# Kernel optimization log

Hardware: AMD Instinct MI355X
Metric: run time of the kernel (lower is better)

## Reference

```python
import jax, jax.numpy as jnp
import numpy as np


def _cd2(a, b):
    # squared euclidean distances [n,m]
    d = jnp.sum(a * a, 1)[:, None] + jnp.sum(b * b, 1)[None, :] - 2.0 * (a @ b.T)
    return jnp.maximum(d, 0.0)


def _cdist(a, b):
    # tiny clamp keeps sqrt grad finite on the zero diagonal, fwd unchanged
    return jnp.sqrt(jnp.maximum(_cd2(a, b), 1e-30))


def _tmedian(x):
    # torch.median semantics: lower middle element
    f = jnp.sort(x.reshape(-1))
    return f[(f.shape[0] - 1) // 2]


def setup_inputs() -> dict:
    key = jax.random.key(0)
    k1, k2 = jax.random.split(key)
    feat_s = jax.random.normal(k1, (25, 640), dtype=jnp.float32)
    y_s = (jnp.arange(25) % 5).astype(jnp.int32)  # 5-way 5-shot, every class present
    feat_q = jax.random.normal(k2, (300, 640), dtype=jnp.float32)
    return {"feat_s": feat_s, "y_s": y_s, "feat_q": feat_q}


def reference(feat_s, y_s, feat_q):
    y_s_np = np.asarray(y_s)
    classes = np.unique(y_s_np)
    C = int(classes.shape[0])
    onehot = jnp.asarray(y_s_np[:, None] == classes[None, :], dtype=feat_s.dtype)  # [S,C]
    prototypes = (onehot.T @ feat_s) / jnp.sum(onehot, 0)[:, None]  # [C,D]

    # ---- virtual mixup densification ----
    dist_q = _cdist(feat_q, prototypes)  # [Nq,C]
    y_boot = np.asarray(jnp.argmin(dist_q, 1))
    q_norm = feat_q / jnp.linalg.norm(feat_q, axis=1, keepdims=True)
    cos_np = np.asarray(q_norm @ q_norm.T)
    dist_q_np = np.asarray(dist_q)
    virt = []
    for c in range(C):
        idx = np.flatnonzero(y_boot == c)
        if idx.size < 2:
            continue
        cos_c = cos_np[np.ix_(idx, idx)]
        f = np.sort(cos_c.reshape(-1))
        thresh = f[(f.size - 1) // 2]  # torch lower median
        ii, jj = np.nonzero(np.triu(cos_c >= thresh, 1))  # pairs with i<j
        if ii.size:
            virt.append(0.5 * (feat_q[idx[ii]] + feat_q[idx[jj]]))
        kq = int(idx[np.argmin(dist_q_np[idx, c])])
        virt.append((0.5 * (prototypes[c] + feat_q[kq]))[None, :])
    feat_all = jnp.concatenate([feat_q] + virt, 0) if virt else feat_q

    # ---- self-tuning affinity (kNN graph) ----
    n = int(feat_all.shape[0])
    k = max(1, int(np.log2(n)))
    dist = _cdist(feat_all, feat_all)  # [n,n]
    _, nn_idx = jax.lax.top_k(-dist, k + 1)  # smallest k+1 (incl. self)
    sigma = dist[jnp.arange(n), nn_idx[:, k]] + 1e-8
    nbrs = nn_idx[:, 1:]  # [n,k]
    d_nb = jnp.take_along_axis(dist, nbrs, 1)
    w = jnp.exp(-d_nb / (sigma[:, None] * sigma[nbrs]))
    W = jnp.zeros((n, n), feat_all.dtype).at[jnp.arange(n)[:, None], nbrs].set(w)
    W = (W + W.T) / 2
    D_inv = 1.0 / (W.sum(1) + 1e-8)

    # ---- density-adaptive lambda ----
    d = _cdist(feat_all, prototypes).min(1)
    lam = jnp.exp(-(d ** 2) / (2 * _tmedian(d) ** 2 + 1e-8))

    # ---- mm iterations (label propagation) ----
    a = _cd2(feat_all, prototypes)  # [n,C]
    y0 = jax.nn.softmax(-a, axis=1)
    scale = (lam * D_inv)[:, None]

    def step(carry, _):
        y, done = carry
        y_new = jax.nn.softmax(-a + scale * (W @ y), axis=1)
        conv = jnp.max(jnp.abs(y_new - y)) < 1e-4
        y_out = jnp.where(done | conv, y, y_new)  # emulate torch early break
        return (y_out, done | conv), None

    (y, _), _ = jax.lax.scan(step, (y0, jnp.asarray(False)), None, length=50)
    preds = jnp.argmax(y[: feat_q.shape[0]], 1)
    return preds
```

## Files before the change

### kernel.cpp

```cpp
#include <hip/hip_runtime.h>
#include <math.h>

#define CMAX 8
#define KMAX 16
#define TPB 256
#define BNMAX 1024

struct P {
  const float* fs; const int* ys; const float* fq;
  int S, Q, D, BN, NMAX;
  float* proto;
  float* G;
  float* cosq;
  int* ybt;
  int* cls; int* scount; int* qcount; int* qidx; int* kq;
  float* thr;
  int* rowcnt; int* rowoff; int* paircnt; int* basev;
  int* meta;
  int* uv;
  float* rn2;
  float* H;
  int* cand;
  int* nbrs; float* dnb; float* wgt; float* sigma;
  int* indeg; int* inoff; int* cursor;
  int* insrcU; float* inwU; int* indst;
  int* insrc; float* inw;
  unsigned* cosk;
  unsigned* gmaxu;
  float* amat; float* dinv; float* dmin; float* scalev;
  float* yA; float* yB;
  float* meddenom;
  int* outp;
};

__device__ inline unsigned f2key(float f){
  unsigned b=__float_as_uint(f);
  return (b&0x80000000u)? ~b : (b|0x80000000u);
}
__device__ inline float key2f(unsigned k){
  unsigned b=(k&0x80000000u)? (k^0x80000000u) : ~k;
  return __uint_as_float(b);
}
__device__ inline unsigned long long shfl_xor_u64(unsigned long long v,int m){
  unsigned lo=(unsigned)v, hi=(unsigned)(v>>32);
  lo=__shfl_xor(lo,m,64); hi=__shfl_xor(hi,m,64);
  return (((unsigned long long)hi)<<32)|lo;
}

__global__ void k_init(P p){
  if (threadIdx.x==0){
    int labs[CMAX]; int cnt[CMAX]; int C=0;
    for (int s=0;s<p.S;s++){
      int l=p.ys[s]; int f=-1;
      for(int c=0;c<C;c++) if(labs[c]==l){f=c;break;}
      if(f<0){ if(C<CMAX){labs[C]=l;cnt[C]=1;C++;} }
      else cnt[f]++;
    }
    for(int a=0;a<C;a++)for(int b=a+1;b<C;b++)
      if(labs[b]<labs[a]){int t=labs[a];labs[a]=labs[b];labs[b]=t;
                          t=cnt[a];cnt[a]=cnt[b];cnt[b]=t;}
    for(int c=0;c<C;c++){p.cls[c]=labs[c];p.scount[c]=cnt[c];}
    p.meta[0]=C;
  }
}

__global__ void k_proto(P p){
  int c=blockIdx.x; int C=p.meta[0];
  for(int d=threadIdx.x; d<p.D; d+=blockDim.x){
    float s=0.f;
    if(c<C){
      int lab=p.cls[c];
      for(int j=0;j<p.S;j++) if(p.ys[j]==lab) s+=p.fs[(size_t)j*p.D+d];
      s/= (float)p.scount[c];
    }
    p.proto[(size_t)c*p.D+d]=s;
  }
}

__global__ void k_gram(P p){
  __shared__ float arow[1024];
  int a=blockIdx.x;
  const float* ra = (a<p.Q)? p.fq + (size_t)a*p.D : p.proto + (size_t)(a-p.Q)*p.D;
  const float* A = ra;
  if(p.D<=1024){
    for(int d=threadIdx.x; d<p.D; d+=blockDim.x) arow[d]=ra[d];
    __syncthreads();
    A=(const float*)arow;
  }
  int D4=p.D>>2; int Dt=D4<<2;
  for(int b=threadIdx.x; b<p.BN; b+=blockDim.x){
    const float* rb=(b<p.Q)? p.fq+(size_t)b*p.D : p.proto+(size_t)(b-p.Q)*p.D;
    const float4* a4=(const float4*)A;
    const float4* b4=(const float4*)rb;
    float s=0.f;
    #pragma unroll 4
    for(int d=0;d<D4;d++){
      float4 x=a4[d], y=b4[d];
      s += x.x*y.x + x.y*y.y + x.z*y.z + x.w*y.w;
    }
    for(int d=Dt;d<p.D;d++) s += A[d]*rb[d];
    p.G[(size_t)a*p.BN+b]=s;
  }
}

__global__ void k_cos(P p){
  int t=blockIdx.x*blockDim.x+threadIdx.x;
  if(t>=p.Q*p.Q)return;
  int i=t/p.Q, j=t%p.Q;
  p.cosq[t]=p.G[(size_t)i*p.BN+j]/(sqrtf(p.G[(size_t)i*p.BN+i])*sqrtf(p.G[(size_t)j*p.BN+j]));
}

__global__ void k_yboot(P p){
  int q=blockIdx.x*blockDim.x+threadIdx.x;
  if(q>=p.Q)return;
  int C=p.meta[0];
  float gq=p.G[(size_t)q*p.BN+q];
  float best=INFINITY; int bc=0;
  for(int c=0;c<C;c++){
    int pc=p.Q+c;
    float d2=gq+p.G[(size_t)pc*p.BN+pc]-2.f*p.G[(size_t)q*p.BN+pc];
    d2=fmaxf(d2,0.f);
    if(d2<best){best=d2;bc=c;}
  }
  p.ybt[q]=bc;
}

__global__ void k_qidx(P p){
  int c=blockIdx.x; int C=p.meta[0];
  int lane=threadIdx.x;
  if(c>=C){ if(lane==0){p.qcount[c]=0;p.kq[c]=0;} return; }
  int base=0;
  for(int q0=0;q0<p.Q;q0+=64){
    int q=q0+lane;
    bool in = (q<p.Q) && (p.ybt[q]==c);
    unsigned long long mask=__ballot(in);
    int pre=__popcll(mask & ((lane==63)?0x7FFFFFFFFFFFFFFFull:((1ull<<lane)-1ull)));
    if(in) p.qidx[c*p.Q+base+pre]=q;
    base+=__popcll(mask);
  }
  if(lane==0) p.qcount[c]=base;
  int pc=p.Q+c;
  float gp=p.G[(size_t)pc*p.BN+pc];
  unsigned long long best=0xFFFFFFFFFFFFFFFFull;
  for(int t=lane;t<base;t+=64){
    int q=p.qidx[c*p.Q+t];
    float d2=fmaxf(p.G[(size_t)q*p.BN+q]+gp-2.f*p.G[(size_t)q*p.BN+pc],0.f);
    unsigned long long key=(((unsigned long long)f2key(d2))<<32)|(unsigned)t;
    if(key<best)best=key;
  }
  #pragma unroll
  for(int s=32;s>=1;s>>=1){
    unsigned long long o=shfl_xor_u64(best,s);
    if(o<best)best=o;
  }
  if(lane==0){
    int t=(int)(unsigned)(best&0xFFFFFFFFull);
    p.kq[c]=(base>0)? p.qidx[c*p.Q+t] : 0;
  }
}

__global__ void k_median(P p){
  __shared__ unsigned hist[256];
  __shared__ unsigned sPref; __shared__ int sTrem;
  __shared__ int sqidx[512];
  int c=blockIdx.x; int C=p.meta[0];
  int m=(c<C)? p.qcount[c]:0;
  int tid=threadIdx.x;
  if(m<2){ if(tid==0) p.thr[c]=INFINITY; return; }
  const int* qix;
  if(p.Q<=512){
    for(int t=tid;t<m;t+=blockDim.x) sqidx[t]=p.qidx[c*p.Q+t];
    __syncthreads();
    qix=sqidx;
  } else qix=p.qidx+c*p.Q;
  int total=m*m;
  unsigned* keys=p.cosk+(size_t)c*p.Q*p.Q;
  for(int t=tid;t<total;t+=blockDim.x){
    int a=t/m, b=t-a*m;
    keys[t]=f2key(p.cosq[(size_t)qix[a]*p.Q+qix[b]]);
  }
  if(tid==0){ sPref=0u; sTrem=(total-1)/2; }
  __syncthreads();
  unsigned prefmask=0u;
  for(int shift=24;shift>=0;shift-=8){
    hist[tid&255]=0u;
    __syncthreads();
    unsigned pref=sPref;
    for(int t=tid;t<total;t+=blockDim.x){
      unsigned key=keys[t];
      if((key&prefmask)==pref) atomicAdd(&hist[(key>>shift)&255],1u);
    }
    __syncthreads();
    if(tid==0){
      int trem=sTrem; unsigned cum=0;
      for(int b=0;b<256;b++){
        unsigned h=hist[b];
        if(cum+h>(unsigned)trem){ sPref=pref|((unsigned)b<<shift); sTrem=trem-(int)cum; break; }
        cum+=h;
      }
    }
    __syncthreads();
    prefmask|=(0xFFu<<shift);
  }
  if(tid==0) p.thr[c]=key2f(sPref);
}

__global__ void k_rowcnt(P p){
  int c=blockIdx.x; int C=p.meta[0];
  int m=(c<C)? p.qcount[c]:0;
  if(m<2){ if(threadIdx.x==0) p.paircnt[c]=0; return; }
  float th=p.thr[c];
  for(int a=threadIdx.x;a<m;a+=blockDim.x){
    int ia=p.qidx[c*p.Q+a]; int cnt=0;
    const float* row=p.cosq+(size_t)ia*p.Q;
    for(int b=a+1;b<m;b++){
      int ib=p.qidx[c*p.Q+b];
      cnt += (row[ib]>=th);
    }
    p.rowcnt[c*p.Q+a]=cnt;
  }
  __syncthreads();
  if(threadIdx.x==0){
    int run=0;
    for(int a=0;a<m;a++){p.rowoff[c*p.Q+a]=run; run+=p.rowcnt[c*p.Q+a];}
    p.paircnt[c]=run;
  }
}

__global__ void k_bases(P p){
  int C=p.meta[0]; int cur=p.Q;
  for(int c=0;c<C;c++){
    p.basev[c]=cur;
    if(p.qcount[c]>=2) cur += p.paircnt[c]+1;
  }
  int n=cur; if(n>p.NMAX)n=p.NMAX;
  p.meta[1]=n;
  int k=31-__clz(n); if(k<1)k=1; if(k>KMAX-1)k=KMAX-1;
  p.meta[2]=k;
  p.meta[3]=0;
  p.meta[4]=0;
  p.meta[5]=0;
  for(int t=0;t<64;t++) p.gmaxu[t]=0u;
}

__global__ void k_uv(P p){
  int r=blockIdx.x*blockDim.x+threadIdx.x;
  if(r>=p.NMAX)return;
  p.indeg[r]=0;
  if(r<p.Q){ p.uv[2*r]=r; p.uv[2*r+1]=r; }
}

__global__ void k_uvpairs(P p){
  int c=blockIdx.x; int C=p.meta[0];
  int m=(c<C)? p.qcount[c]:0;
  if(m<2)return;
  float th=p.thr[c];
  int bs=p.basev[c];
  for(int a=threadIdx.x;a<m;a+=blockDim.x){
    int ia=p.qidx[c*p.Q+a];
    int off=bs+p.rowoff[c*p.Q+a]; int cnt=0;
    const float* row=p.cosq+(size_t)ia*p.Q;
    for(int b=a+1;b<m;b++){
      int ib=p.qidx[c*p.Q+b];
      if(row[ib]>=th){
        int r=off+cnt;
        p.uv[2*r]=ia; p.uv[2*r+1]=ib;
        cnt++;
      }
    }
  }
  if(threadIdx.x==0){
    int r=bs+p.paircnt[c];
    p.uv[2*r]=p.Q+c; p.uv[2*r+1]=p.kq[c];
  }
}

__global__ void k_hrow(P p){
  int i=blockIdx.x;
  int n=p.meta[1]; if(i>=n)return;
  int u=p.uv[2*i], v=p.uv[2*i+1];
  const float* Gu=p.G+(size_t)u*p.BN;
  const float* Gv=p.G+(size_t)v*p.BN;
  float* h=p.H+(size_t)i*p.BN;
  for(int x=threadIdx.x;x<p.BN;x+=64) h[x]=0.5f*(Gu[x]+Gv[x]);
  __syncthreads();
  if(threadIdx.x==0){
    float rn=0.5f*(h[u]+h[v]);
    p.rn2[i]=rn;
    ((int4*)p.cand)[i]=make_int4(u,v,__float_as_int(rn),0);
  }
}

template<int KSEL>
__device__ void knn_body(const P& p,int i,int n,int kp1,const float* sh,float rni){
  int lane=threadIdx.x;
  unsigned long long r[KSEL];
  #pragma unroll
  for(int t=0;t<KSEL;t++) r[t]=0xFFFFFFFFFFFFFFFFull;
  unsigned long long thrw=0xFFFFFFFFFFFFFFFFull;
  int iters=(n+63)>>6;
  const int4* cand=(const int4*)p.cand;
  for(int it=0;it<iters;++it){
    int j=(it<<6)+lane;
    unsigned long long key=0xFFFFFFFFFFFFFFFFull;
    if(j<n){
      int4 cd=cand[j];
      float d2=fmaxf(rni+__int_as_float(cd.z)-sh[cd.x]-sh[cd.y],0.f);
      key=(((unsigned long long)f2key(d2))<<32)|(unsigned)j;
    }
    if(key<thrw && key<r[KSEL-1]){
      #pragma unroll
      for(int t=0;t<KSEL;t++){
        bool lt=key<r[t];
        unsigned long long lo=lt?key:r[t];
        unsigned long long hi=lt?r[t]:key;
        r[t]=lo; key=hi;
      }
    }
    if((it&15)==15){
      unsigned long long v=r[KSEL-1];
      #pragma unroll
      for(int s=32;s>=1;s>>=1){
        unsigned long long o=shfl_xor_u64(v,s);
        if(o<v)v=o;
      }
      thrw=v;
    }
  }
  for(int t=0;t<kp1;t++){
    unsigned long long m=r[0];
    #pragma unroll
    for(int s=32;s>=1;s>>=1){
      unsigned long long o=shfl_xor_u64(m,s);
      if(o<m)m=o;
    }
    if(r[0]==m){
      #pragma unroll
      for(int q=0;q<KSEL-1;q++) r[q]=r[q+1];
      r[KSEL-1]=0xFFFFFFFFFFFFFFFFull;
    }
    if(lane==0){
      int j=(int)(unsigned)(m&0xFFFFFFFFull);
      float d2=key2f((unsigned)(m>>32));
      float dd=sqrtf(fmaxf(d2,1e-30f));
      if(t>=1){ p.nbrs[(size_t)i*KMAX+t-1]=j; p.dnb[(size_t)i*KMAX+t-1]=dd; }
      if(t==kp1-1) p.sigma[i]=dd+1e-8f;
    }
  }
}

__global__ void k_knn(P p){
  __shared__ float sh[BNMAX];
  int i=blockIdx.x;
  int n=p.meta[1]; if(i>=n)return;
  int kp1=p.meta[2]+1;
  const float* h=p.H+(size_t)i*p.BN;
  const float* hp=h;
  if(p.BN<=BNMAX){
    for(int d=threadIdx.x;d<p.BN;d+=64) sh[d]=h[d];
    __syncthreads();
    hp=(const float*)sh;
  }
  float rni=p.rn2[i];
  if(kp1<=13) knn_body<13>(p,i,n,kp1,hp,rni);
  else        knn_body<16>(p,i,n,kp1,hp,rni);
}

__global__ void k_wgtcnt(P p){
  int i=blockIdx.x*blockDim.x+threadIdx.x;
  int n=p.meta[1]; if(i>=n)return;
  int k=p.meta[2];
  float si=p.sigma[i];
  for(int q=0;q<k;q++){
    int j=p.nbrs[(size_t)i*KMAX+q];
    p.wgt[(size_t)i*KMAX+q]=expf(-p.dnb[(size_t)i*KMAX+q]/(si*p.sigma[j]));
    atomicAdd(&p.indeg[j],1);
  }
  for(int q=k;q<KMAX;q++){ p.nbrs[(size_t)i*KMAX+q]=i; p.wgt[(size_t)i*KMAX+q]=0.f; }
}

__global__ void k_scan(P p){
  __shared__ int part[TPB];
  int n=p.meta[1];
  int chunk=(n+TPB-1)/TPB;
  int beg=threadIdx.x*chunk, end=beg+chunk; if(end>n)end=n;
  int s=0;
  for(int i=beg;i<end;i++) s+=p.indeg[i];
  part[threadIdx.x]=s; __syncthreads();
  if(threadIdx.x==0){
    int run=0;
    for(int t=0;t<TPB;t++){int v=part[t];part[t]=run;run+=v;}
    p.inoff[n]=run;
  }
  __syncthreads();
  int run=part[threadIdx.x];
  for(int i=beg;i<end;i++){
    p.inoff[i]=run; p.cursor[i]=run; run+=p.indeg[i];
  }
}

__global__ void k_fill(P p){
  int i=blockIdx.x*blockDim.x+threadIdx.x;
  int n=p.meta[1]; if(i>=n)return;
  int k=p.meta[2];
  for(int q=0;q<k;q++){
    int dst=p.nbrs[(size_t)i*KMAX+q];
    int slot=atomicAdd(&p.cursor[dst],1);
    p.insrcU[slot]=i; p.inwU[slot]=p.wgt[(size_t)i*KMAX+q]; p.indst[slot]=dst;
  }
}

__global__ void k_rank(P p){
  int e=blockIdx.x*blockDim.x+threadIdx.x;
  int n=p.meta[1];
  int E=p.inoff[n];
  if(e>=E)return;
  int dst=p.indst[e];
  int b=p.inoff[dst], en=p.inoff[dst+1];
  int s=p.insrcU[e]; float w=p.inwU[e];
  int rank=0;
  for(int x=b;x<en;x++) rank += (p.insrcU[x]<s);
  p.insrc[b+rank]=s; p.inw[b+rank]=w;
}

__global__ void k_dad(P p){
  int i=blockIdx.x*blockDim.x+threadIdx.x;
  int n=p.meta[1]; if(i>=n)return;
  int k=p.meta[2]; int C=p.meta[0];
  float s=0.f;
  for(int q=0;q<k;q++) s+=p.wgt[(size_t)i*KMAX+q];
  for(int e=p.inoff[i];e<p.inoff[i+1];e++) s+=p.inw[e];
  p.dinv[i]=1.f/(0.5f*s+1e-8f);
  int u=p.uv[2*i],v=p.uv[2*i+1];
  float rn=p.rn2[i]; float mn=INFINITY;
  #pragma unroll
  for(int c=0;c<CMAX;c++){
    float a=INFINITY;
    if(c<C){
      int pc=p.Q+c;
      a=rn+p.G[(size_t)pc*p.BN+pc]-(p.G[(size_t)u*p.BN+pc]+p.G[(size_t)v*p.BN+pc]);
      a=fmaxf(a,0.f);
      mn=fminf(mn,a);
    }
    p.amat[(size_t)i*CMAX+c]=a;
  }
  p.dmin[i]=sqrtf(fmaxf(mn,1e-30f));
}

__global__ void k_medd(P p){
  __shared__ unsigned hist[256];
  __shared__ unsigned sPref; __shared__ int sTrem;
  int n=p.meta[1];
  int tid=threadIdx.x;
  if(tid==0){ sPref=0u; sTrem=(n-1)/2; }
  __syncthreads();
  unsigned prefmask=0u;
  for(int shift=24;shift>=0;shift-=8){
    hist[tid&255]=0u;
    __syncthreads();
    unsigned pref=sPref;
    for(int i=tid;i<n;i+=blockDim.x){
      unsigned key=f2key(p.dmin[i]);
      if((key&prefmask)==pref) atomicAdd(&hist[(key>>shift)&255],1u);
    }
    __syncthreads();
    if(tid==0){
      int trem=sTrem; unsigned cum=0;
      for(int b=0;b<256;b++){
        unsigned h=hist[b];
        if(cum+h>(unsigned)trem){ sPref=pref|((unsigned)b<<shift); sTrem=trem-(int)cum; break; }
        cum+=h;
      }
    }
    __syncthreads();
    prefmask|=(0xFFu<<shift);
  }
  if(tid==0){
    float med=key2f(sPref);
    p.meddenom[0]=2.f*med*med+1e-8f;
  }
}

__global__ void k_y0(P p){
  int i=blockIdx.x*blockDim.x+threadIdx.x;
  int n=p.meta[1]; if(i>=n)return;
  float la=expf(-(p.dmin[i]*p.dmin[i])/p.meddenom[0]);
  p.scalev[i]=la*p.dinv[i];
  float mn=INFINITY;
  #pragma unroll
  for(int c=0;c<CMAX;c++) mn=fminf(mn,p.amat[(size_t)i*CMAX+c]);
  float ex[CMAX]; float sum=0.f;
  #pragma unroll
  for(int c=0;c<CMAX;c++){
    float e=expf(mn-p.amat[(size_t)i*CMAX+c]);
    ex[c]=e; sum+=e;
  }
  float inv=1.f/sum;
  #pragma unroll
  for(int c=0;c<CMAX;c++) p.yA[(size_t)i*CMAX+c]=ex[c]*inv;
}

__global__ void k_step(P p,int t){
  if(p.meta[3]) return;
  int n=p.meta[1];
  int par=p.meta[4];
  float* cur=par? p.yB : p.yA;
  float* nxt=par? p.yA : p.yB;
  int i=blockIdx.x*blockDim.x+threadIdx.x;
  float dmx=0.f;
  if(i<n){
    float wax=0,way=0,waz=0,waw=0,wbx=0,wby=0,wbz=0,wbw=0;
    #pragma unroll
    for(int q=0;q<KMAX;q++){
      int j=p.nbrs[(size_t)i*KMAX+q];
      float w=p.wgt[(size_t)i*KMAX+q];
      const float4* yr=(const float4*)(cur+(size_t)j*CMAX);
      float4 y0=yr[0],y1=yr[1];
      wax+=w*y0.x; way+=w*y0.y; waz+=w*y0.z; waw+=w*y0.w;
      wbx+=w*y1.x; wby+=w*y1.y; wbz+=w*y1.z; wbw+=w*y1.w;
    }
    int e1=p.inoff[i+1];
    for(int e=p.inoff[i];e<e1;e++){
      int j=p.insrc[e]; float w=p.inw[e];
      const float4* yr=(const float4*)(cur+(size_t)j*CMAX);
      float4 y0=yr[0],y1=yr[1];
      wax+=w*y0.x; way+=w*y0.y; waz+=w*y0.z; waw+=w*y0.w;
      wbx+=w*y1.x; wby+=w*y1.y; wbz+=w*y1.z; wbw+=w*y1.w;
    }
    float sc=p.scalev[i]*0.5f;
    const float4* am=(const float4*)(p.amat+(size_t)i*CMAX);
    float4 a0=am[0],a1=am[1];
    float l0=sc*wax-a0.x, l1=sc*way-a0.y, l2=sc*waz-a0.z, l3=sc*waw-a0.w;
    float l4=sc*wbx-a1.x, l5=sc*wby-a1.y, l6=sc*wbz-a1.z, l7=sc*wbw-a1.w;
    float mx=fmaxf(fmaxf(fmaxf(l0,l1),fmaxf(l2,l3)),fmaxf(fmaxf(l4,l5),fmaxf(l6,l7)));
    float x0=expf(l0-mx),x1=expf(l1-mx),x2=expf(l2-mx),x3=expf(l3-mx);
    float x4=expf(l4-mx),x5=expf(l5-mx),x6=expf(l6-mx),x7=expf(l7-mx);
    float inv=1.f/(x0+x1+x2+x3+x4+x5+x6+x7);
    float4 o0=make_float4(x0*inv,x1*inv,x2*inv,x3*inv);
    float4 o1=make_float4(x4*inv,x5*inv,x6*inv,x7*inv);
    const float4* cr=(const float4*)(cur+(size_t)i*CMAX);
    float4 c0=cr[0],c1=cr[1];
    dmx=fmaxf(dmx,fabsf(o0.x-c0.x)); dmx=fmaxf(dmx,fabsf(o0.y-c0.y));
    dmx=fmaxf(dmx,fabsf(o0.z-c0.z)); dmx=fmaxf(dmx,fabsf(o0.w-c0.w));
    dmx=fmaxf(dmx,fabsf(o1.x-c1.x)); dmx=fmaxf(dmx,fabsf(o1.y-c1.y));
    dmx=fmaxf(dmx,fabsf(o1.z-c1.z)); dmx=fmaxf(dmx,fabsf(o1.w-c1.w));
    float4* nr=(float4*)(nxt+(size_t)i*CMAX);
    nr[0]=o0; nr[1]=o1;
  }
  #pragma unroll
  for(int s=32;s>=1;s>>=1) dmx=fmaxf(dmx,__shfl_xor(dmx,s,64));
  if(threadIdx.x==0){
    atomicMax(p.gmaxu+t,__float_as_uint(dmx));
    __threadfence();
    int fin=atomicAdd(&p.meta[5],1);
    if(fin==(int)gridDim.x-1){
      p.meta[5]=0;
      float mm=__uint_as_float(p.gmaxu[t]);
      if(mm<1e-4f) p.meta[3]=1;
      else         p.meta[4]=par^1;
    }
  }
}

__global__ void k_arg(P p){
  int q=blockIdx.x*blockDim.x+threadIdx.x;
  if(q>=p.Q)return;
  int C=p.meta[0];
  const float* cur=p.meta[4]? p.yB : p.yA;
  float best=cur[(size_t)q*CMAX+0]; int bc=0;
  for(int c=1;c<C;c++){
    float v=cur[(size_t)q*CMAX+c];
    if(v>best){best=v;bc=c;}
  }
  p.outp[q]=bc;
}


static void make_layout(char* base,int S,int Q,int D,int BN,long N,
                        const float*fs,const int*ys,const float*fq,
                        int* outp, P* pp, size_t* need){
  size_t off=0;
  auto A=[&](size_t b)->char*{
    size_t o=(off+255)&~(size_t)255; off=o+b; return base+o;
  };
  P p{};
  p.fs=fs;p.ys=ys;p.fq=fq;p.S=S;p.Q=Q;p.D=D;p.BN=BN;p.NMAX=(int)N;
  p.proto=(float*)A(4ul*CMAX*D);
  p.G=(float*)A(4ul*(size_t)BN*BN);
  p.cosq=(float*)A(4ul*(size_t)Q*Q);
  p.ybt=(int*)A(4ul*Q);
  p.cls=(int*)A(4ul*CMAX);
  p.scount=(int*)A(4ul*CMAX);
  p.qcount=(int*)A(4ul*CMAX);
  p.qidx=(int*)A(4ul*CMAX*Q);
  p.kq=(int*)A(4ul*CMAX);
  p.thr=(float*)A(4ul*CMAX);
  p.rowcnt=(int*)A(4ul*CMAX*Q);
  p.rowoff=(int*)A(4ul*CMAX*Q);
  p.paircnt=(int*)A(4ul*CMAX);
  p.basev=(int*)A(4ul*CMAX);
  p.meta=(int*)A(4ul*16);
  p.uv=(int*)A(8ul*N);
  p.rn2=(float*)A(4ul*N);
  p.H=(float*)A(4ul*(size_t)N*BN);
  p.cand=(int*)A(16ul*N);
  p.nbrs=(int*)A(4ul*KMAX*N);
  p.dnb=(float*)A(4ul*KMAX*N);
  p.wgt=(float*)A(4ul*KMAX*N);
  p.sigma=(float*)A(4ul*N);
  p.indeg=(int*)A(4ul*N);
  p.inoff=(int*)A(4ul*(N+1));
  p.cursor=(int*)A(4ul*N);
  p.insrcU=(int*)A(4ul*KMAX*N);
  p.inwU=(float*)A(4ul*KMAX*N);
  p.indst=(int*)A(4ul*KMAX*N);
  p.insrc=(int*)A(4ul*KMAX*N);
  p.inw=(float*)A(4ul*KMAX*N);
  p.cosk=(unsigned*)A(4ul*CMAX*(size_t)Q*Q);
  p.gmaxu=(unsigned*)A(4ul*64);
  p.amat=(float*)A(4ul*CMAX*N);
  p.dinv=(float*)A(4ul*N);
  p.dmin=(float*)A(4ul*N);
  p.scalev=(float*)A(4ul*N);
  p.yA=(float*)A(4ul*CMAX*N);
  p.yB=(float*)A(4ul*CMAX*N);
  p.meddenom=(float*)A(4ul*4);
  p.outp=outp;
  *pp=p; *need=off;
}

extern "C" void kernel_launch(void* const* d_in, const int* in_sizes, int n_in,
                              void* d_out, int out_size, void* d_ws, size_t ws_size,
                              hipStream_t stream){
  const float* fs=(const float*)d_in[0];
  const int*   ys=(const int*)d_in[1];
  const float* fq=(const float*)d_in[2];
  int S=in_sizes[1];
  int D=in_sizes[0]/S;
  int Q=in_sizes[2]/D;
  int BN=Q+CMAX;

  long full=(long)Q + (long)Q*(Q-1)/2 + CMAX;
  long cand[4]={full,16384,8192,5000};
  P p{}; size_t need=0; int NMAX=(int)cand[3];
  for(int ci=0;ci<4;ci++){
    long N=cand[ci]; if(N<Q+CMAX)N=Q+CMAX;
    make_layout((char*)d_ws,S,Q,D,BN,N,fs,ys,fq,(int*)d_out,&p,&need);
    NMAX=(int)N;
    if(need<=ws_size) break;
  }

  int gN=(NMAX+TPB-1)/TPB;
  long gEl=((long)NMAX*KMAX+TPB-1)/TPB;
  int gE=(int)gEl;
  int gS=(NMAX+63)/64;

  k_init   <<<1, 64, 0, stream>>>(p);
  k_proto  <<<CMAX, TPB, 0, stream>>>(p);
  k_gram   <<<BN, TPB, 0, stream>>>(p);
  k_cos    <<<(Q*Q+TPB-1)/TPB, TPB, 0, stream>>>(p);
  k_yboot  <<<(Q+TPB-1)/TPB, TPB, 0, stream>>>(p);
  k_qidx   <<<CMAX, 64, 0, stream>>>(p);
  k_median <<<CMAX, TPB, 0, stream>>>(p);
  k_rowcnt <<<CMAX, TPB, 0, stream>>>(p);
  k_bases  <<<1, 1, 0, stream>>>(p);
  k_uv     <<<gN, TPB, 0, stream>>>(p);
  k_uvpairs<<<CMAX, TPB, 0, stream>>>(p);
  k_hrow   <<<NMAX, 64, 0, stream>>>(p);
  k_knn    <<<NMAX, 64, 0, stream>>>(p);
  k_wgtcnt <<<gN, TPB, 0, stream>>>(p);
  k_scan   <<<1, TPB, 0, stream>>>(p);
  k_fill   <<<gN, TPB, 0, stream>>>(p);
  k_rank   <<<gE, TPB, 0, stream>>>(p);
  k_dad    <<<gN, TPB, 0, stream>>>(p);
  k_medd   <<<1, TPB, 0, stream>>>(p);
  k_y0     <<<gN, TPB, 0, stream>>>(p);
  for(int t=0;t<50;t++)
    k_step <<<gS, 64, 0, stream>>>(p, t);
  k_arg    <<<(Q+TPB-1)/TPB, TPB, 0, stream>>>(p);
}
```

Measured before the change: 603.6 us.

## Fuse H-row build into kNN, split kNN over two waves, 4 lanes per row in step

Drops the materialised H buffer and the k_hrow kernel. The kNN kernel now builds each H row directly in shared memory from two Gram rows, and a small kernel computes the rn2/cand values. The kNN selection uses 128 threads, with two waves each keeping a 32-bit key/index top-k list, and the two lists are merged serially at the end. The label-propagation step assigns 4 lanes per node, with partial sums reduced by shuffles, and reduces atomics to one per wave, which cuts per-thread latency in the 50 repeated launches. The tie-breaking semantics of the key change slightly, and the larger grid adds some overhead per launch.

New measurement: 604.4 us. About the same (+0.1%).

```diff
diff --git a/kernel.cpp b/kernel.cpp
--- a/kernel.cpp
+++ b/kernel.cpp
@@ -19,7 +19,6 @@
   int* meta;
   int* uv;
   float* rn2;
-  float* H;
   int* cand;
   int* nbrs; float* dnb; float* wgt; float* sigma;
   int* indeg; int* inoff; int* cursor;
@@ -275,71 +274,101 @@
   }
 }
 
-__global__ void k_hrow(P p){
-  int i=blockIdx.x;
-  int n=p.meta[1]; if(i>=n)return;
-  int u=p.uv[2*i], v=p.uv[2*i+1];
-  const float* Gu=p.G+(size_t)u*p.BN;
-  const float* Gv=p.G+(size_t)v*p.BN;
-  float* h=p.H+(size_t)i*p.BN;
-  for(int x=threadIdx.x;x<p.BN;x+=64) h[x]=0.5f*(Gu[x]+Gv[x]);
-  __syncthreads();
-  if(threadIdx.x==0){
-    float rn=0.5f*(h[u]+h[v]);
-    p.rn2[i]=rn;
-    ((int4*)p.cand)[i]=make_int4(u,v,__float_as_int(rn),0);
-  }
+__global__ void k_rn2c(P p){
+  int r=blockIdx.x*blockDim.x+threadIdx.x;
+  int n=p.meta[1]; if(r>=n)return;
+  int u=p.uv[2*r],v=p.uv[2*r+1];
+  float hu=0.5f*(p.G[(size_t)u*p.BN+u]+p.G[(size_t)v*p.BN+u]);
+  float hv=0.5f*(p.G[(size_t)u*p.BN+v]+p.G[(size_t)v*p.BN+v]);
+  float rn=0.5f*(hu+hv);
+  p.rn2[r]=rn;
+  ((int4*)p.cand)[r]=make_int4(u,v,__float_as_int(rn),0);
 }
 
 template<int KSEL>
-__device__ void knn_body(const P& p,int i,int n,int kp1,const float* sh,float rni){
-  int lane=threadIdx.x;
-  unsigned long long r[KSEL];
+__device__ void knn_scan(const P& p,int n,int kp1,const float* sh,bool useSh,
+                         const float* Gu,const float* Gv,float rni,
+                         unsigned long long* wl){
+  int lane=threadIdx.x&63; int w=threadIdx.x>>6;
+  unsigned kf[KSEL]; int kj[KSEL];
   #pragma unroll
-  for(int t=0;t<KSEL;t++) r[t]=0xFFFFFFFFFFFFFFFFull;
-  unsigned long long thrw=0xFFFFFFFFFFFFFFFFull;
-  int iters=(n+63)>>6;
+  for(int t=0;t<KSEL;t++){ kf[t]=0xFFFFFFFFu; kj[t]=0x7FFFFFFF; }
+  unsigned thrw=0xFFFFFFFFu;
+  int iters=(n+127)>>7;
   const int4* cand=(const int4*)p.cand;
   for(int it=0;it<iters;++it){
-    int j=(it<<6)+lane;
-    unsigned long long key=0xFFFFFFFFFFFFFFFFull;
+    int j=(it<<7)+(w<<6)+lane;
+    unsigned key=0xFFFFFFFFu;
     if(j<n){
       int4 cd=cand[j];
-      float d2=fmaxf(rni+__int_as_float(cd.z)-sh[cd.x]-sh[cd.y],0.f);
-      key=(((unsigned long long)f2key(d2))<<32)|(unsigned)j;
-    }
-    if(key<thrw && key<r[KSEL-1]){
+      float dot = useSh ? (sh[cd.x]+sh[cd.y])
+                        : 0.5f*(Gu[cd.x]+Gv[cd.x])+0.5f*(Gu[cd.y]+Gv[cd.y]);
+      float d2=fmaxf(rni+__int_as_float(cd.z)-dot,0.f);
+      key=f2key(d2);
+    }
+    if(key<=thrw && key<kf[KSEL-1]){
+      int cj=j;
       #pragma unroll
       for(int t=0;t<KSEL;t++){
-        bool lt=key<r[t];
-        unsigned long long lo=lt?key:r[t];
-        unsigned long long hi=lt?r[t]:key;
-        r[t]=lo; key=hi;
+        bool lt = key<kf[t];
+        unsigned nk = lt? key : kf[t];
+        unsigned ok = lt? kf[t] : key;
+        int nj = lt? cj : kj[t];
+        int oj = lt? kj[t] : cj;
+        kf[t]=nk; kj[t]=nj; key=ok; cj=oj;
       }
     }
-    if((it&15)==15){
-      unsigned long long v=r[KSEL-1];
+    if((it&7)==7){
+      unsigned v=kf[KSEL-1];
       #pragma unroll
       for(int s=32;s>=1;s>>=1){
-        unsigned long long o=shfl_xor_u64(v,s);
+        unsigned o=(unsigned)__shfl_xor((int)v,s,64);
         if(o<v)v=o;
       }
       thrw=v;
     }
   }
   for(int t=0;t<kp1;t++){
-    unsigned long long m=r[0];
+    unsigned long long mv=(((unsigned long long)kf[0])<<32)|(unsigned)kj[0];
+    unsigned long long m=mv;
     #pragma unroll
     for(int s=32;s>=1;s>>=1){
       unsigned long long o=shfl_xor_u64(m,s);
       if(o<m)m=o;
     }
-    if(r[0]==m){
+    if(mv==m){
       #pragma unroll
-      for(int q=0;q<KSEL-1;q++) r[q]=r[q+1];
-      r[KSEL-1]=0xFFFFFFFFFFFFFFFFull;
-    }
-    if(lane==0){
+      for(int q=0;q<KSEL-1;q++){ kf[q]=kf[q+1]; kj[q]=kj[q+1]; }
+      kf[KSEL-1]=0xFFFFFFFFu; kj[KSEL-1]=0x7FFFFFFF;
+    }
+    if(lane==0) wl[w*16+t]=m;
+  }
+}
+
+__global__ void __launch_bounds__(128) k_knn(P p){
+  __shared__ float sh[BNMAX];
+  __shared__ unsigned long long wl[32];
+  int i=blockIdx.x;
+  int n=p.meta[1]; if(i>=n)return;
+  int kp1=p.meta[2]+1;
+  int u1=p.uv[2*i], v1=p.uv[2*i+1];
+  const float* Gu=p.G+(size_t)u1*p.BN;
+  const float* Gv=p.G+(size_t)v1*p.BN;
+  bool useSh=(p.BN<=BNMAX);
+  if(useSh){
+    for(int d=threadIdx.x; d<p.BN; d+=128) sh[d]=0.5f*(Gu[d]+Gv[d]);
+  }
+  __syncthreads();
+  float rni=p.rn2[i];
+  if(kp1<=13) knn_scan<13>(p,n,kp1,sh,useSh,Gu,Gv,rni,wl);
+  else        knn_scan<16>(p,n,kp1,sh,useSh,Gu,Gv,rni,wl);
+  __syncthreads();
+  if(threadIdx.x==0){
+    int a=0,b=0;
+    for(int t=0;t<kp1;t++){
+      unsigned long long va=wl[a], vb=wl[16+b];
+      unsigned long long m;
+      if(va<=vb){m=va;a++;} else {m=vb;b++;}
       int j=(int)(unsigned)(m&0xFFFFFFFFull);
       float d2=key2f((unsigned)(m>>32));
       float dd=sqrtf(fmaxf(d2,1e-30f));
@@ -347,23 +376,6 @@
       if(t==kp1-1) p.sigma[i]=dd+1e-8f;
     }
   }
-}
-
-__global__ void k_knn(P p){
-  __shared__ float sh[BNMAX];
-  int i=blockIdx.x;
-  int n=p.meta[1]; if(i>=n)return;
-  int kp1=p.meta[2]+1;
-  const float* h=p.H+(size_t)i*p.BN;
-  const float* hp=h;
-  if(p.BN<=BNMAX){
-    for(int d=threadIdx.x;d<p.BN;d+=64) sh[d]=h[d];
-    __syncthreads();
-    hp=(const float*)sh;
-  }
-  float rni=p.rn2[i];
-  if(kp1<=13) knn_body<13>(p,i,n,kp1,hp,rni);
-  else        knn_body<16>(p,i,n,kp1,hp,rni);
 }
 
 __global__ void k_wgtcnt(P p){
@@ -500,18 +512,20 @@
   for(int c=0;c<CMAX;c++) p.yA[(size_t)i*CMAX+c]=ex[c]*inv;
 }
 
-__global__ void k_step(P p,int t){
+__global__ void __launch_bounds__(256) k_step(P p,int t){
   if(p.meta[3]) return;
   int n=p.meta[1];
   int par=p.meta[4];
   float* cur=par? p.yB : p.yA;
   float* nxt=par? p.yA : p.yB;
-  int i=blockIdx.x*blockDim.x+threadIdx.x;
+  int gt=blockIdx.x*blockDim.x+threadIdx.x;
+  int i=gt>>2; int sub=gt&3;
   float dmx=0.f;
   if(i<n){
     float wax=0,way=0,waz=0,waw=0,wbx=0,wby=0,wbz=0,wbw=0;
     #pragma unroll
-    for(int q=0;q<KMAX;q++){
+    for(int m=0;m<4;m++){
+      int q=sub+4*m;
       int j=p.nbrs[(size_t)i*KMAX+q];
       float w=p.wgt[(size_t)i*KMAX+q];
       const float4* yr=(const float4*)(cur+(size_t)j*CMAX);
@@ -520,12 +534,19 @@
       wbx+=w*y1.x; wby+=w*y1.y; wbz+=w*y1.z; wbw+=w*y1.w;
     }
     int e1=p.inoff[i+1];
-    for(int e=p.inoff[i];e<e1;e++){
+    for(int e=p.inoff[i]+sub;e<e1;e+=4){
       int j=p.insrc[e]; float w=p.inw[e];
       const float4* yr=(const float4*)(cur+(size_t)j*CMAX);
       float4 y0=yr[0],y1=yr[1];
       wax+=w*y0.x; way+=w*y0.y; waz+=w*y0.z; waw+=w*y0.w;
       wbx+=w*y1.x; wby+=w*y1.y; wbz+=w*y1.z; wbw+=w*y1.w;
+    }
+    #pragma unroll
+    for(int m=1;m<=2;m<<=1){
+      wax+=__shfl_xor(wax,m,64); way+=__shfl_xor(way,m,64);
+      waz+=__shfl_xor(waz,m,64); waw+=__shfl_xor(waw,m,64);
+      wbx+=__shfl_xor(wbx,m,64); wby+=__shfl_xor(wby,m,64);
+      wbz+=__shfl_xor(wbz,m,64); wbw+=__shfl_xor(wbw,m,64);
     }
     float sc=p.scalev[i]*0.5f;
     const float4* am=(const float4*)(p.amat+(size_t)i*CMAX);
@@ -538,19 +559,22 @@
     float inv=1.f/(x0+x1+x2+x3+x4+x5+x6+x7);
     float4 o0=make_float4(x0*inv,x1*inv,x2*inv,x3*inv);
     float4 o1=make_float4(x4*inv,x5*inv,x6*inv,x7*inv);
-    const float4* cr=(const float4*)(cur+(size_t)i*CMAX);
-    float4 c0=cr[0],c1=cr[1];
-    dmx=fmaxf(dmx,fabsf(o0.x-c0.x)); dmx=fmaxf(dmx,fabsf(o0.y-c0.y));
-    dmx=fmaxf(dmx,fabsf(o0.z-c0.z)); dmx=fmaxf(dmx,fabsf(o0.w-c0.w));
-    dmx=fmaxf(dmx,fabsf(o1.x-c1.x)); dmx=fmaxf(dmx,fabsf(o1.y-c1.y));
-    dmx=fmaxf(dmx,fabsf(o1.z-c1.z)); dmx=fmaxf(dmx,fabsf(o1.w-c1.w));
-    float4* nr=(float4*)(nxt+(size_t)i*CMAX);
-    nr[0]=o0; nr[1]=o1;
+    if(sub==0){
+      const float4* cr=(const float4*)(cur+(size_t)i*CMAX);
+      float4 c0=cr[0],c1=cr[1];
+      dmx=fmaxf(dmx,fabsf(o0.x-c0.x)); dmx=fmaxf(dmx,fabsf(o0.y-c0.y));
+      dmx=fmaxf(dmx,fabsf(o0.z-c0.z)); dmx=fmaxf(dmx,fabsf(o0.w-c0.w));
+      dmx=fmaxf(dmx,fabsf(o1.x-c1.x)); dmx=fmaxf(dmx,fabsf(o1.y-c1.y));
+      dmx=fmaxf(dmx,fabsf(o1.z-c1.z)); dmx=fmaxf(dmx,fabsf(o1.w-c1.w));
+      float4* nr=(float4*)(nxt+(size_t)i*CMAX);
+      nr[0]=o0; nr[1]=o1;
+    }
   }
   #pragma unroll
   for(int s=32;s>=1;s>>=1) dmx=fmaxf(dmx,__shfl_xor(dmx,s,64));
+  if((threadIdx.x&63)==0) atomicMax(p.gmaxu+t,__float_as_uint(dmx));
+  __syncthreads();
   if(threadIdx.x==0){
-    atomicMax(p.gmaxu+t,__float_as_uint(dmx));
     __threadfence();
     int fin=atomicAdd(&p.meta[5],1);
     if(fin==(int)gridDim.x-1){
@@ -602,7 +626,6 @@
   p.meta=(int*)A(4ul*16);
   p.uv=(int*)A(8ul*N);
   p.rn2=(float*)A(4ul*N);
-  p.H=(float*)A(4ul*(size_t)N*BN);
   p.cand=(int*)A(16ul*N);
   p.nbrs=(int*)A(4ul*KMAX*N);
   p.dnb=(float*)A(4ul*KMAX*N);
@@ -666,8 +689,8 @@
   k_bases  <<<1, 1, 0, stream>>>(p);
   k_uv     <<<gN, TPB, 0, stream>>>(p);
   k_uvpairs<<<CMAX, TPB, 0, stream>>>(p);
-  k_hrow   <<<NMAX, 64, 0, stream>>>(p);
-  k_knn    <<<NMAX, 64, 0, stream>>>(p);
+  k_rn2c   <<<gN, TPB, 0, stream>>>(p);
+  k_knn    <<<NMAX, 128, 0, stream>>>(p);
   k_wgtcnt <<<gN, TPB, 0, stream>>>(p);
   k_scan   <<<1, TPB, 0, stream>>>(p);
   k_fill   <<<gN, TPB, 0, stream>>>(p);
@@ -676,6 +699,6 @@
   k_medd   <<<1, TPB, 0, stream>>>(p);
   k_y0     <<<gN, TPB, 0, stream>>>(p);
   for(int t=0;t<50;t++)
-    k_step <<<gS, 64, 0, stream>>>(p, t);
+    k_step <<<gS, 256, 0, stream>>>(p, t);
   k_arg    <<<(Q+TPB-1)/TPB, TPB, 0, stream>>>(p);
 }
```
